# Kernel optimization log

Hardware: AMD Instinct MI355X
Metric: run time of the kernel (lower is better)

Reference implementation:

```python
import jax, jax.numpy as jnp
import numpy as np

N_NODES = 500000   # total temporal-graph nodes (memory slots)
N_SUB = 50000      # nodes in sampled subgraph (|n_id|)
E = 500000         # edges from LastNeighborLoader (N_SUB * neighbor_size)
B = 5000           # events in the batch
D = 100            # memory_dim == embedding_dim
TD = 100           # time_dim
MSG = 100          # msg_dim
H = 2              # TransformerConv heads
C = D // H         # per-head channels
OUT = 100          # predictor out_channels


def setup_inputs() -> dict:
    key = jax.random.key(0)
    ks = jax.random.split(key, 32)
    s = 0.1
    r = lambda i, shp: jax.random.normal(ks[i], shp, dtype=jnp.float32) * s
    return {
        'memory': r(0, (N_NODES, D)),
        'last_update': jax.random.randint(ks[1], (N_NODES,), 0, 1000000, dtype=jnp.int32),
        'n_id': jax.random.randint(ks[2], (N_SUB,), 0, N_NODES, dtype=jnp.int32),
        'edge_index': jax.random.randint(ks[3], (2, E), 0, N_SUB, dtype=jnp.int32),
        't': jax.random.randint(ks[4], (E,), 0, 1000000, dtype=jnp.int32),
        'msg': r(5, (E, MSG)),
        'src_idx': jax.random.randint(ks[6], (B,), 0, N_SUB, dtype=jnp.int32),
        'dst_idx': jax.random.randint(ks[7], (B,), 0, N_SUB, dtype=jnp.int32),
        'w_time': r(8, (TD, 1)), 'b_time': r(9, (TD,)),
        'Wq': r(10, (D, H * C)), 'bq': r(11, (H * C,)),
        'Wk': r(12, (D, H * C)), 'bk': r(13, (H * C,)),
        'Wv': r(14, (D, H * C)), 'bv': r(15, (H * C,)),
        'We': r(16, (MSG + TD, H * C)),
        'Wskip': r(17, (D, H * C)), 'bskip': r(18, (H * C,)),
        'Wps': r(19, (D, D)), 'bps': r(20, (D,)),
        'Wpd': r(21, (D, D)), 'bpd': r(22, (D,)),
        'Wpf': r(23, (D, OUT)), 'bpf': r(24, (OUT,)),
    }


def reference(memory, last_update, n_id, edge_index, t, msg, src_idx, dst_idx,
              w_time, b_time, Wq, bq, Wk, bk, Wv, bv, We, Wskip, bskip,
              Wps, bps, Wpd, bpd, Wpf, bpf):
    # --- memory lookup: z, last_update = memory(n_id) ---
    z = memory[n_id]                       # [N_SUB, D] gather
    lu = last_update[n_id]                 # [N_SUB]

    src = edge_index[0]
    dst = edge_index[1]

    # --- relative time encoding: cos(Linear(1, time_dim)) ---
    rel_t = (lu[src] - t).astype(jnp.float32)              # [E]
    rel_t_enc = jnp.cos(rel_t[:, None] * w_time[:, 0][None, :] + b_time)  # [E, TD]
    edge_attr = jnp.concatenate([rel_t_enc, msg], axis=-1)  # [E, TD+MSG]

    # --- TransformerConv (heads=H, per-head C, edge_dim, root skip) ---
    q = (z @ Wq + bq).reshape(N_SUB, H, C)
    k = (z @ Wk + bk).reshape(N_SUB, H, C)
    v = (z @ Wv + bv).reshape(N_SUB, H, C)
    e = (edge_attr @ We).reshape(E, H, C)

    key_e = k[src] + e                     # [E, H, C]
    val_e = v[src] + e                     # [E, H, C]
    alpha = jnp.sum(q[dst] * key_e, axis=-1) / jnp.sqrt(jnp.float32(C))  # [E, H]

    # segment softmax over incoming edges of each dst node
    m = jax.ops.segment_max(alpha, dst, num_segments=N_SUB)   # [N_SUB, H]
    a = jnp.exp(alpha - m[dst])
    denom = jax.ops.segment_sum(a, dst, num_segments=N_SUB)
    a = a / (denom[dst] + 1e-16)

    agg = jax.ops.segment_sum(a[:, :, None] * val_e, dst, num_segments=N_SUB)  # [N_SUB, H, C]
    out = agg.reshape(N_SUB, H * C) + (z @ Wskip + bskip)     # [N_SUB, D]

    # --- predictor on src/dst embeddings (assoc remap already applied) ---
    h = jax.nn.relu((out[src_idx] @ Wps + bps) + (out[dst_idx] @ Wpd + bpd))
    pred = h @ Wpf + bpf                   # [B, OUT]
    return pred
```

## Files before the change

kernel.cpp:

```cpp
#include <hip/hip_runtime.h>
#include <math.h>

#define N_SUBN  50000
#define NE      500000
#define NB      5000
#define NL      (2*NB)
#define DDIM    100
#define TDIM    100
#define KATTR   200
#define NCHUNK  49

typedef __attribute__((ext_vector_type(8))) short short8;
typedef __attribute__((ext_vector_type(4))) float f32x4;

__device__ inline unsigned short f2bf(float f){
  union{float f; unsigned int u;} v; v.f = f;
  unsigned int r = (v.u + 0x7fffu + ((v.u >> 16) & 1u)) >> 16;
  return (unsigned short)r;
}
__device__ inline float bf2f(unsigned short u){
  union{unsigned int u; float f;} v; v.u = ((unsigned int)u) << 16;
  return v.f;
}

__device__ inline float fast_cos(float x){
  constexpr double TWO_PI_D = 6.2831853071795864769252867665590;
  constexpr float I2PI = (float)(1.0/TWO_PI_D);
  constexpr float C1 = (float)TWO_PI_D;
  constexpr float C2 = (float)(TWO_PI_D - (double)((float)TWO_PI_D));
  float k = rintf(x * I2PI);
  float r = fmaf(k, -C1, x);
  r = fmaf(k, -C2, r);
  return __cosf(r);
}

__global__ __launch_bounds__(256) void k_misc(
    const int* __restrict__ lastu, const int* __restrict__ nid,
    int* __restrict__ cnt, int* __restrict__ mark, int* __restrict__ lusub,
    const float* __restrict__ We,
    const float* __restrict__ Wq, const float* __restrict__ Wk,
    const float* __restrict__ Wv, const float* __restrict__ Ws,
    const float* __restrict__ Wps, const float* __restrict__ Wpd,
    const float* __restrict__ Wpf,
    unsigned short* __restrict__ Wnb, unsigned short* __restrict__ Wqxb,
    unsigned short* __restrict__ Wfb)
{
  int i = blockIdx.x*256 + threadIdx.x;
  if (i < N_SUBN){
    cnt[i] = 0;
    mark[i] = 0;
    lusub[i] = lastu[nid[i]];
  }
  if (i < 7*28*64){
    int l = i & 63; int t = i >> 6;
    int which = t / 28; int t2 = t - which*28;
    int kt = t2 / 7; int nt = t2 - kt*7;
    const float* W = (which==0)?Wq:(which==1)?Wk:(which==2)?Wv:(which==3)?Ws:
                     (which==4)?Wps:(which==5)?Wpd:Wpf;
    int col = nt*16 + (l & 15);
    int kbase = kt*32 + ((l >> 4) << 3);
    short8 pack;
    #pragma unroll
    for (int j = 0; j < 8; ++j){
      int k = kbase + j;
      float v = (k < DDIM && col < DDIM) ? W[k*DDIM + col] : 0.f;
      pack[j] = (short)f2bf(v);
    }
    *((short8*)Wnb + i) = pack;
  }
  if (i < 4*25*64){
    int l = i & 63; int t = i >> 6;
    int kt = t / 25; int nt = t - kt*25;
    int col = nt*16 + (l & 15);
    int h = col / 200; int d = col - h*200;
    int kbase = kt*32 + ((l >> 4) << 3);
    short8 pack;
    #pragma unroll
    for (int j = 0; j < 8; ++j){
      int k = kbase + j;
      float v = (k >= h*50 && k < h*50 + 50) ? We[d*DDIM + k] : 0.f;
      pack[j] = (short)f2bf(v);
    }
    *((short8*)Wqxb + i) = pack;
  }
  if (i < 13*7*64){
    int l = i & 63; int t = i >> 6;
    int kt = t / 7; int nt = t - kt*7;
    int col = nt*16 + (l & 15);
    int kbase = kt*32 + ((l >> 4) << 3);
    short8 pack;
    #pragma unroll
    for (int j = 0; j < 8; ++j){
      int k = kbase + j;
      float v = 0.f;
      if (col < DDIM && k < 2*KATTR){
        int h = col / 50; int blk = k / KATTR; int d = k - blk*KATTR;
        v = (blk == h) ? We[d*DDIM + col] : 0.f;
      }
      pack[j] = (short)f2bf(v);
    }
    *((short8*)Wfb + i) = pack;
  }
}

__global__ void k_mark(const int* __restrict__ srci, const int* __restrict__ dsti,
                       int* __restrict__ mark){
  int i = blockIdx.x*blockDim.x + threadIdx.x;
  if (i < NB){
    mark[srci[i]] = 1;
    mark[dsti[i]] = 1;
  }
}

__global__ void k_hist(const int* __restrict__ ei, const int* __restrict__ mark,
                       int* __restrict__ cnt){
  int i = blockIdx.x*blockDim.x + threadIdx.x;
  if (i < NE){
    int d = ei[NE + i];
    if (mark[d]) atomicAdd(&cnt[d], 1);
  }
}

__global__ __launch_bounds__(256) void k_bsum(const int* __restrict__ cnt, int* __restrict__ bsum){
  __shared__ int wsum[4];
  int b = blockIdx.x, tid = threadIdx.x;
  int base = b*1024 + tid*4;
  int s = 0;
  #pragma unroll
  for (int i=0;i<4;i++){ int idx = base+i; if (idx < N_SUBN) s += cnt[idx]; }
  #pragma unroll
  for (int m=1;m<64;m<<=1) s += __shfl_xor(s, m);
  if ((tid&63)==0) wsum[tid>>6] = s;
  __syncthreads();
  if (tid==0) bsum[b] = wsum[0]+wsum[1]+wsum[2]+wsum[3];
}

__global__ void k_bscan(const int* __restrict__ bsum, int* __restrict__ bbase){
  int l = threadIdx.x;
  int v = (l < NCHUNK) ? bsum[l] : 0;
  int orig = v;
  for (int off=1; off<64; off<<=1){
    int t = __shfl_up(v, off);
    if (l >= off) v += t;
  }
  if (l < NCHUNK) bbase[l] = v - orig;
}

__global__ __launch_bounds__(1024) void k_off(const int* __restrict__ cnt, const int* __restrict__ bbase,
                                              int* __restrict__ rowptr, int* __restrict__ ofs){
  __shared__ int sd[1024];
  int b = blockIdx.x, tid = threadIdx.x;
  int i = b*1024 + tid;
  int v = (i < N_SUBN) ? cnt[i] : 0;
  sd[tid] = v; __syncthreads();
  for (int off=1; off<1024; off<<=1){
    int t = (tid >= off) ? sd[tid-off] : 0;
    __syncthreads();
    sd[tid] += t;
    __syncthreads();
  }
  int incl = sd[tid] + bbase[b];
  if (i < N_SUBN){ rowptr[i+1] = incl; ofs[i] = incl - v; }
  if (i == 0) rowptr[0] = 0;
}

__global__ void k_perm(const int* __restrict__ ei, const int* __restrict__ tt,
                       const int* __restrict__ lusub, const int* __restrict__ mark,
                       int* __restrict__ ofs, uint4* __restrict__ spr){
  int i = blockIdx.x*blockDim.x + threadIdx.x;
  if (i < NE){
    int d = ei[NE + i];
    if (mark[d]){
      int s = ei[i];
      float rel = (float)(lusub[s] - tt[i]);
      int pos = atomicAdd(&ofs[d], 1);
      spr[pos] = make_uint4((unsigned)s, (unsigned)i, __float_as_uint(rel), 0u);
    }
  }
}

__global__ __launch_bounds__(256, 4) void k_nodeKV(
    const float* __restrict__ mem, const int* __restrict__ nid,
    const unsigned short* __restrict__ Wnb,
    const float* __restrict__ bk, const float* __restrict__ bv,
    unsigned short* __restrict__ kvb)
{
  const int tid = threadIdx.x;
  const int lane = tid & 63;
  const int w = tid >> 6;
  const int node0 = blockIdx.x*64;
  const int arow = w*16 + (lane & 15);
  const int koff = (lane >> 4) << 3;

  int node = node0 + arow;
  int nc = (node < N_SUBN) ? node : (N_SUBN-1);
  const float* zrow = mem + (size_t)nid[nc]*DDIM;

  f32x4 ak[7], av[7];
  #pragma unroll
  for (int nt=0; nt<7; ++nt){ ak[nt] = (f32x4){0,0,0,0}; av[nt] = (f32x4){0,0,0,0}; }

  #pragma unroll
  for (int kt=0; kt<4; ++kt){
    const int k0 = kt*32 + koff;
    short8 a;
    if (k0 + 7 < DDIM){
      float4 m0 = *(const float4*)(zrow + k0);
      float4 m1 = *(const float4*)(zrow + k0 + 4);
      a[0] = (short)f2bf(m0.x); a[1] = (short)f2bf(m0.y);
      a[2] = (short)f2bf(m0.z); a[3] = (short)f2bf(m0.w);
      a[4] = (short)f2bf(m1.x); a[5] = (short)f2bf(m1.y);
      a[6] = (short)f2bf(m1.z); a[7] = (short)f2bf(m1.w);
    } else if (k0 >= DDIM){
      #pragma unroll
      for (int j=0;j<8;++j) a[j] = 0;
    } else {
      float4 m0 = *(const float4*)(zrow + 96);
      a[0] = (short)f2bf(m0.x); a[1] = (short)f2bf(m0.y);
      a[2] = (short)f2bf(m0.z); a[3] = (short)f2bf(m0.w);
      a[4] = 0; a[5] = 0; a[6] = 0; a[7] = 0;
    }
    const short8* wk = (const short8*)Wnb + (size_t)((1*4 + kt)*7)*64 + lane;
    const short8* wv = (const short8*)Wnb + (size_t)((2*4 + kt)*7)*64 + lane;
    #pragma unroll
    for (int nt=0; nt<7; ++nt){
      ak[nt] = __builtin_amdgcn_mfma_f32_16x16x32_bf16(a, wk[(size_t)nt*64], ak[nt], 0, 0, 0);
      av[nt] = __builtin_amdgcn_mfma_f32_16x16x32_bf16(a, wv[(size_t)nt*64], av[nt], 0, 0, 0);
    }
  }

  const int colb = lane & 15;
  const int rbase = w*16 + ((lane >> 4) << 2);
  #pragma unroll
  for (int nt=0; nt<7; ++nt){
    int col = nt*16 + colb;
    if (col >= DDIM) continue;
    float bbk = bk[col], bbv = bv[col];
    #pragma unroll
    for (int r=0; r<4; ++r){
      int nn = node0 + rbase + r;
      if (nn < N_SUBN){
        unsigned pk = (unsigned)f2bf(ak[nt][r] + bbk)
                    | ((unsigned)f2bf(av[nt][r] + bbv) << 16);
        *(unsigned*)(kvb + (size_t)nn*(2*DDIM) + col*2) = pk;
      }
    }
  }
}

__global__ __launch_bounds__(256, 4) void k_nodeQS(
    const float* __restrict__ mem, const int* __restrict__ nid,
    const int* __restrict__ srci, const int* __restrict__ dsti,
    const unsigned short* __restrict__ Wnb,
    const float* __restrict__ bq, const float* __restrict__ bs,
    float* __restrict__ qs, float* __restrict__ ss)
{
  const int tid = threadIdx.x;
  const int lane = tid & 63;
  const int w = tid >> 6;
  const int i0 = blockIdx.x*64;
  const int arow = w*16 + (lane & 15);
  const int koff = (lane >> 4) << 3;

  int idx = i0 + arow;
  int idxc = (idx < NL) ? idx : (NL-1);
  int node = (idxc < NB) ? srci[idxc] : dsti[idxc - NB];
  const float* zrow = mem + (size_t)nid[node]*DDIM;

  f32x4 aq[7], as_[7];
  #pragma unroll
  for (int nt=0; nt<7; ++nt){ aq[nt] = (f32x4){0,0,0,0}; as_[nt] = (f32x4){0,0,0,0}; }

  #pragma unroll
  for (int kt=0; kt<4; ++kt){
    const int k0 = kt*32 + koff;
    short8 a;
    if (k0 + 7 < DDIM){
      float4 m0 = *(const float4*)(zrow + k0);
      float4 m1 = *(const float4*)(zrow + k0 + 4);
      a[0] = (short)f2bf(m0.x); a[1] = (short)f2bf(m0.y);
      a[2] = (short)f2bf(m0.z); a[3] = (short)f2bf(m0.w);
      a[4] = (short)f2bf(m1.x); a[5] = (short)f2bf(m1.y);
      a[6] = (short)f2bf(m1.z); a[7] = (short)f2bf(m1.w);
    } else if (k0 >= DDIM){
      #pragma unroll
      for (int j=0;j<8;++j) a[j] = 0;
    } else {
      float4 m0 = *(const float4*)(zrow + 96);
      a[0] = (short)f2bf(m0.x); a[1] = (short)f2bf(m0.y);
      a[2] = (short)f2bf(m0.z); a[3] = (short)f2bf(m0.w);
      a[4] = 0; a[5] = 0; a[6] = 0; a[7] = 0;
    }
    const short8* wq = (const short8*)Wnb + (size_t)((0*4 + kt)*7)*64 + lane;
    const short8* ws = (const short8*)Wnb + (size_t)((3*4 + kt)*7)*64 + lane;
    #pragma unroll
    for (int nt=0; nt<7; ++nt){
      aq[nt]  = __builtin_amdgcn_mfma_f32_16x16x32_bf16(a, wq[(size_t)nt*64], aq[nt], 0, 0, 0);
      as_[nt] = __builtin_amdgcn_mfma_f32_16x16x32_bf16(a, ws[(size_t)nt*64], as_[nt], 0, 0, 0);
    }
  }

  const int colb = lane & 15;
  const int rbase = w*16 + ((lane >> 4) << 2);
  int nd[4]; bool on[4];
  #pragma unroll
  for (int r=0; r<4; ++r){
    int ii = i0 + rbase + r;
    on[r] = ii < NL;
    int iic = on[r] ? ii : (NL-1);
    nd[r] = (iic < NB) ? srci[iic] : dsti[iic - NB];
  }
  #pragma unroll
  for (int nt=0; nt<7; ++nt){
    int col = nt*16 + colb;
    if (col >= DDIM) continue;
    float bbq = bq[col], bbs = bs[col];
    #pragma unroll
    for (int r=0; r<4; ++r){
      if (on[r]){
        qs[(size_t)nd[r]*DDIM + col] = aq[nt][r] + bbq;
        ss[(size_t)nd[r]*DDIM + col] = as_[nt][r] + bbs;
      }
    }
  }
}

__global__ __launch_bounds__(256) void k_qex(
    const float* __restrict__ qs, const int* __restrict__ srci, const int* __restrict__ dsti,
    const unsigned short* __restrict__ Wqxb, unsigned short* __restrict__ qexb)
{
  const int tid = threadIdx.x;
  const int lane = tid & 63;
  const int w = tid >> 6;
  const int i0 = blockIdx.x*64;
  const int arow = w*16 + (lane & 15);
  const int koff = (lane >> 4) << 3;

  int idx = i0 + arow;
  int idxc = (idx < NL) ? idx : (NL-1);
  int node = (idxc < NB) ? srci[idxc] : dsti[idxc - NB];
  const float* qrow = qs + (size_t)node*DDIM;

  f32x4 acc[25];
  #pragma unroll
  for (int nt=0; nt<25; ++nt) acc[nt] = (f32x4){0,0,0,0};

  #pragma unroll
  for (int kt=0; kt<4; ++kt){
    const int k0 = kt*32 + koff;
    short8 a;
    if (k0 + 7 < DDIM){
      float4 m0 = *(const float4*)(qrow + k0);
      float4 m1 = *(const float4*)(qrow + k0 + 4);
      a[0] = (short)f2bf(m0.x); a[1] = (short)f2bf(m0.y);
      a[2] = (short)f2bf(m0.z); a[3] = (short)f2bf(m0.w);
      a[4] = (short)f2bf(m1.x); a[5] = (short)f2bf(m1.y);
      a[6] = (short)f2bf(m1.z); a[7] = (short)f2bf(m1.w);
    } else if (k0 >= DDIM){
      #pragma unroll
      for (int j=0;j<8;++j) a[j] = 0;
    } else {
      float4 m0 = *(const float4*)(qrow + 96);
      a[0] = (short)f2bf(m0.x); a[1] = (short)f2bf(m0.y);
      a[2] = (short)f2bf(m0.z); a[3] = (short)f2bf(m0.w);
      a[4] = 0; a[5] = 0; a[6] = 0; a[7] = 0;
    }
    const short8* wb = (const short8*)Wqxb + (size_t)(kt*25)*64 + lane;
    #pragma unroll
    for (int nt=0; nt<25; ++nt){
      short8 b = wb[(size_t)nt*64];
      acc[nt] = __builtin_amdgcn_mfma_f32_16x16x32_bf16(a, b, acc[nt], 0, 0, 0);
    }
  }

  const int colb = lane & 15;
  const int rbase = w*16 + ((lane >> 4) << 2);
  int nd[4]; bool on[4];
  #pragma unroll
  for (int r=0; r<4; ++r){
    int ii = i0 + rbase + r;
    on[r] = ii < NL;
    int iic = on[r] ? ii : (NL-1);
    nd[r] = (iic < NB) ? srci[iic] : dsti[iic - NB];
  }
  #pragma unroll
  for (int nt=0; nt<25; ++nt){
    int col = nt*16 + colb;
    #pragma unroll
    for (int r=0; r<4; ++r){
      if (on[r]) qexb[(size_t)nd[r]*400 + col] = f2bf(acc[nt][r]);
    }
  }
}

__global__ __launch_bounds__(256) void k_agg(
    const int* __restrict__ rowptr, const uint4* __restrict__ spr,
    const int* __restrict__ srci, const int* __restrict__ dsti,
    const float* __restrict__ msg, const float* __restrict__ qs,
    const unsigned short* __restrict__ qexb, const unsigned short* __restrict__ kvb,
    const float* __restrict__ wt, const float* __restrict__ bt,
    unsigned short* __restrict__ sbarb, float* __restrict__ numvb,
    float* __restrict__ denb)
{
  const int w = __builtin_amdgcn_readfirstlane(threadIdx.x >> 6);
  const int lane = threadIdx.x & 63;
  const int idx = blockIdx.x*4 + w;
  const int node = (idx < NB) ? srci[idx] : dsti[idx - NB];
  const bool act = lane < 50;
  const int l = lane;
  const float INV = 0.14142135623730951f;

  float wtA=0,wtB=0,btA=0,btB=0,q0=0,q1=0;
  float qx0=0,qx1=0,qx2=0,qx3=0,qx4=0,qx5=0,qx6=0,qx7=0;
  if (act){
    wtA = wt[l]; wtB = wt[50+l]; btA = bt[l]; btB = bt[50+l];
    q0 = qs[(size_t)node*DDIM + l]; q1 = qs[(size_t)node*DDIM + 50 + l];
    const unsigned short* qe = qexb + (size_t)node*400;
    qx0 = bf2f(qe[l]);      qx1 = bf2f(qe[50+l]);
    qx2 = bf2f(qe[100+l]);  qx3 = bf2f(qe[150+l]);
    qx4 = bf2f(qe[200+l]);  qx5 = bf2f(qe[250+l]);
    qx6 = bf2f(qe[300+l]);  qx7 = bf2f(qe[350+l]);
  }
  const int b0 = rowptr[node], b1 = rowptr[node+1];
  float den0=0.f, den1=0.f, nv0=0.f, nv1=0.f;
  float sb0=0.f,sb1=0.f,sb2=0.f,sb3=0.f,sb4=0.f,sb5=0.f,sb6=0.f,sb7=0.f;

  const int nE = b1 - b0;
  const int npairs = nE >> 1;

  uint4 sA = make_uint4(0,0,0,0), sB = sA, nsA = sA, nsB = sA;
  float mAA=0,mBA=0,mAB=0,mBB=0;
  unsigned pA0=0,pA1=0,pB0=0,pB1=0;

  if (npairs > 0){
    sA = spr[b0]; sB = spr[b0+1];
    if (act){
      mAA = msg[(size_t)sA.y*DDIM + l];  mBA = msg[(size_t)sA.y*DDIM + 50 + l];
      mAB = msg[(size_t)sB.y*DDIM + l];  mBB = msg[(size_t)sB.y*DDIM + 50 + l];
      pA0 = *(const unsigned*)(kvb + (size_t)sA.x*(2*DDIM) + 2*l);
      pA1 = *(const unsigned*)(kvb + (size_t)sA.x*(2*DDIM) + 100 + 2*l);
      pB0 = *(const unsigned*)(kvb + (size_t)sB.x*(2*DDIM) + 2*l);
      pB1 = *(const unsigned*)(kvb + (size_t)sB.x*(2*DDIM) + 100 + 2*l);
    }
    if (npairs > 1){ nsA = spr[b0+2]; nsB = spr[b0+3]; }
  }

  for (int j = 0; j < npairs; ++j){
    float nmAA=0,nmBA=0,nmAB=0,nmBB=0;
    unsigned npA0=0,npA1=0,npB0=0,npB1=0;
    if (j+1 < npairs && act){
      nmAA = msg[(size_t)nsA.y*DDIM + l];  nmBA = msg[(size_t)nsA.y*DDIM + 50 + l];
      nmAB = msg[(size_t)nsB.y*DDIM + l];  nmBB = msg[(size_t)nsB.y*DDIM + 50 + l];
      npA0 = *(const unsigned*)(kvb + (size_t)nsA.x*(2*DDIM) + 2*l);
      npA1 = *(const unsigned*)(kvb + (size_t)nsA.x*(2*DDIM) + 100 + 2*l);
      npB0 = *(const unsigned*)(kvb + (size_t)nsB.x*(2*DDIM) + 2*l);
      npB1 = *(const unsigned*)(kvb + (size_t)nsB.x*(2*DDIM) + 100 + 2*l);
    }
    uint4 nnsA = nsA, nnsB = nsB;
    if (j+2 < npairs){
      nnsA = spr[b0 + 2*(j+2)];
      nnsB = spr[b0 + 2*(j+2) + 1];
    }

    float relA = __uint_as_float(sA.z);
    float relB = __uint_as_float(sB.z);
    float cAA=0,cBA=0,cAB=0,cBB=0;
    float kA0=0,vA0=0,kA1=0,vA1=0,kB0=0,vB0=0,kB1=0,vB1=0;
    if (act){
      kA0 = bf2f((unsigned short)(pA0 & 0xffff)); vA0 = bf2f((unsigned short)(pA0 >> 16));
      kA1 = bf2f((unsigned short)(pA1 & 0xffff)); vA1 = bf2f((unsigned short)(pA1 >> 16));
      kB0 = bf2f((unsigned short)(pB0 & 0xffff)); vB0 = bf2f((unsigned short)(pB0 >> 16));
      kB1 = bf2f((unsigned short)(pB1 & 0xffff)); vB1 = bf2f((unsigned short)(pB1 >> 16));
      cAA = fast_cos(__fadd_rn(__fmul_rn(relA, wtA), btA));
// ... 212 lines not shown
      hl[rbase + r][col] = fmaxf(acc[nt][r] + bbias, 0.f);
  }
  __syncthreads();

  f32x4 ac2[7];
  #pragma unroll
  for (int nt=0; nt<7; ++nt) ac2[nt] = (f32x4){0,0,0,0};

  #pragma unroll
  for (int kt=0; kt<4; ++kt){
    const int k0 = kt*32 + koff;
    short8 a;
    if (k0 + 7 < DDIM){
      float4 h0 = *(const float4*)(&hl[arow][k0]);
      float4 h1 = *(const float4*)(&hl[arow][k0 + 4]);
      a[0]=(short)f2bf(h0.x); a[1]=(short)f2bf(h0.y); a[2]=(short)f2bf(h0.z); a[3]=(short)f2bf(h0.w);
      a[4]=(short)f2bf(h1.x); a[5]=(short)f2bf(h1.y); a[6]=(short)f2bf(h1.z); a[7]=(short)f2bf(h1.w);
    } else if (k0 >= DDIM){
      #pragma unroll
      for (int j=0;j<8;++j) a[j] = 0;
    } else {
      float4 h0 = *(const float4*)(&hl[arow][96]);
      a[0]=(short)f2bf(h0.x); a[1]=(short)f2bf(h0.y); a[2]=(short)f2bf(h0.z); a[3]=(short)f2bf(h0.w);
      a[4]=0; a[5]=0; a[6]=0; a[7]=0;
    }
    const short8* wpf = (const short8*)Wnb + (size_t)((6*4 + kt)*7)*64 + lane;
    #pragma unroll
    for (int nt=0; nt<7; ++nt)
      ac2[nt] = __builtin_amdgcn_mfma_f32_16x16x32_bf16(a, wpf[(size_t)nt*64], ac2[nt], 0, 0, 0);
  }

  #pragma unroll
  for (int nt=0; nt<7; ++nt){
    int col = nt*16 + colb;
    if (col >= DDIM) continue;
    float bb = bpf[col];
    #pragma unroll
    for (int r=0; r<4; ++r){
      int bo = bb0 + rbase + r;
      if (bo < NB) outp[(size_t)bo*DDIM + col] = ac2[nt][r] + bb;
    }
  }
}

extern "C" void kernel_launch(void* const* d_in, const int* in_sizes, int n_in,
                              void* d_out, int out_size, void* d_ws, size_t ws_size,
                              hipStream_t stream)
{
  const float* mem   = (const float*)d_in[0];
  const int*   lastu = (const int*)  d_in[1];
  const int*   nid   = (const int*)  d_in[2];
  const int*   ei    = (const int*)  d_in[3];
  const int*   tt    = (const int*)  d_in[4];
  const float* msg   = (const float*)d_in[5];
  const int*   srci  = (const int*)  d_in[6];
  const int*   dsti  = (const int*)  d_in[7];
  const float* wtime = (const float*)d_in[8];
  const float* btime = (const float*)d_in[9];
  const float* Wq = (const float*)d_in[10]; const float* bq = (const float*)d_in[11];
  const float* Wk = (const float*)d_in[12]; const float* bk = (const float*)d_in[13];
  const float* Wv = (const float*)d_in[14]; const float* bv = (const float*)d_in[15];
  const float* We = (const float*)d_in[16];
  const float* Ws = (const float*)d_in[17]; const float* bs = (const float*)d_in[18];
  const float* Wps= (const float*)d_in[19]; const float* bps= (const float*)d_in[20];
  const float* Wpd= (const float*)d_in[21]; const float* bpd= (const float*)d_in[22];
  const float* Wpf= (const float*)d_in[23]; const float* bpf= (const float*)d_in[24];

  char* wsp = (char*)d_ws;
  auto alloc = [&](size_t bytes)->void*{
    void* p = (void*)wsp;
    wsp += (bytes + 255) & ~(size_t)255;
    return p;
  };
  float* qs   = (float*)alloc((size_t)N_SUBN*DDIM*4);
  unsigned short* kvb  = (unsigned short*)alloc((size_t)N_SUBN*DDIM*2*2);
  float* ssb  = (float*)alloc((size_t)N_SUBN*DDIM*4);
  float* oute = (float*)alloc((size_t)N_SUBN*DDIM*4);
  unsigned short* qexb = (unsigned short*)alloc((size_t)N_SUBN*400*2);
  unsigned short* sbarb= (unsigned short*)alloc((size_t)N_SUBN*400*2);
  float* numvb= (float*)alloc((size_t)N_SUBN*DDIM*4);
  float* denb = (float*)alloc((size_t)N_SUBN*2*4);
  int* cnt    = (int*)alloc((size_t)N_SUBN*4);
  int* mark   = (int*)alloc((size_t)N_SUBN*4);
  int* rowptr = (int*)alloc((size_t)(N_SUBN+1)*4);
  int* ofs    = (int*)alloc((size_t)N_SUBN*4);
  int* bsum   = (int*)alloc((size_t)NCHUNK*4);
  int* bbase  = (int*)alloc((size_t)NCHUNK*4);
  uint4* spr  = (uint4*)alloc((size_t)NE*16);
  int* lusub  = (int*)alloc((size_t)N_SUBN*4);
  unsigned short* Wnb  = (unsigned short*)alloc((size_t)7*28*64*8*2);
  unsigned short* Wqxb = (unsigned short*)alloc((size_t)4*25*64*8*2);
  unsigned short* Wfb  = (unsigned short*)alloc((size_t)13*7*64*8*2);

  k_misc<<<(N_SUBN+255)/256, 256, 0, stream>>>(lastu, nid, cnt, mark, lusub, We,
                                               Wq, Wk, Wv, Ws, Wps, Wpd, Wpf,
                                               Wnb, Wqxb, Wfb);
  k_mark<<<(NB+255)/256, 256, 0, stream>>>(srci, dsti, mark);
  k_hist<<<(NE+255)/256, 256, 0, stream>>>(ei, mark, cnt);
  k_bsum<<<NCHUNK, 256, 0, stream>>>(cnt, bsum);
  k_bscan<<<1, 64, 0, stream>>>(bsum, bbase);
  k_off<<<NCHUNK, 1024, 0, stream>>>(cnt, bbase, rowptr, ofs);
  k_perm<<<(NE+255)/256, 256, 0, stream>>>(ei, tt, lusub, mark, ofs, spr);

  k_nodeKV<<<(N_SUBN+63)/64, 256, 0, stream>>>(mem, nid, Wnb, bk, bv, kvb);
  k_nodeQS<<<(NL+63)/64, 256, 0, stream>>>(mem, nid, srci, dsti, Wnb, bq, bs, qs, ssb);
  k_qex<<<(NL+63)/64, 256, 0, stream>>>(qs, srci, dsti, Wqxb, qexb);

  k_agg<<<NL/4, 256, 0, stream>>>(rowptr, spr, srci, dsti, msg, qs,
                                  qexb, kvb, wtime, btime,
                                  sbarb, numvb, denb);

  k_final<<<(NL+63)/64, 256, 0, stream>>>(sbarb, Wfb, srci, dsti, numvb, denb, ssb, oute);

  k_pred<<<(NB+63)/64, 256, 0, stream>>>(oute, srci, dsti, Wnb, bps, bpd, bpf,
                                         (float*)d_out);
}
```

Before: 145.1 us.

## Fold Wq into We projection, skip unneeded KV nodes, merge scan kernels

Precomputes the product of Wq and the per-head We slices, plus a combined bias, so the query-times-edge-weight projection is computed straight from memory rows. This fuses the q/skip projection and the qex projection into one kernel. It also marks source nodes of edges that feed batch destinations, and skips the memory loads and K/V stores for all other nodes. The separate block-scan kernel is removed by having each k_off block sum the preceding block totals itself. The trade-offs are fewer launches and less gather traffic against a serial 50-term dot product per element in the setup kernel and higher register pressure in the fused kernel.

```diff
diff --git a/kernel.cpp b/kernel.cpp
--- a/kernel.cpp
+++ b/kernel.cpp
@@ -36,19 +36,21 @@
 
 __global__ __launch_bounds__(256) void k_misc(
     const int* __restrict__ lastu, const int* __restrict__ nid,
-    int* __restrict__ cnt, int* __restrict__ mark, int* __restrict__ lusub,
+    int* __restrict__ cnt, int* __restrict__ mark, int* __restrict__ mark2,
+    int* __restrict__ lusub,
     const float* __restrict__ We,
     const float* __restrict__ Wq, const float* __restrict__ Wk,
     const float* __restrict__ Wv, const float* __restrict__ Ws,
     const float* __restrict__ Wps, const float* __restrict__ Wpd,
-    const float* __restrict__ Wpf,
-    unsigned short* __restrict__ Wnb, unsigned short* __restrict__ Wqxb,
-    unsigned short* __restrict__ Wfb)
+    const float* __restrict__ Wpf, const float* __restrict__ bq,
+    unsigned short* __restrict__ Wnb, unsigned short* __restrict__ Wqxcb,
+    unsigned short* __restrict__ Wfb, float* __restrict__ bcomb)
 {
   int i = blockIdx.x*256 + threadIdx.x;
   if (i < N_SUBN){
     cnt[i] = 0;
     mark[i] = 0;
+    mark2[i] = 0;
     lusub[i] = lastu[nid[i]];
   }
   if (i < 7*28*64){
@@ -76,12 +78,25 @@
     int kbase = kt*32 + ((l >> 4) << 3);
     short8 pack;
     #pragma unroll
-    for (int j = 0; j < 8; ++j){
-      int k = kbase + j;
-      float v = (k >= h*50 && k < h*50 + 50) ? We[d*DDIM + k] : 0.f;
-      pack[j] = (short)f2bf(v);
-    }
-    *((short8*)Wqxb + i) = pack;
+    for (int j8 = 0; j8 < 8; ++j8){
+      int k = kbase + j8;
+      float v = 0.f;
+      if (k < DDIM){
+        const float* wqr = Wq + k*DDIM + h*50;
+        const float* wer = We + d*DDIM + h*50;
+        for (int j = 0; j < 50; ++j) v = fmaf(wqr[j], wer[j], v);
+      }
+      pack[j8] = (short)f2bf(v);
+    }
+    *((short8*)Wqxcb + i) = pack;
+  }
+  if (i < 400){
+    int h = i / 200; int d = i - h*200;
+    const float* wer = We + d*DDIM + h*50;
+    const float* bqr = bq + h*50;
+    float v = 0.f;
+    for (int j = 0; j < 50; ++j) v = fmaf(bqr[j], wer[j], v);
+    bcomb[i] = v;
   }
   if (i < 13*7*64){
     int l = i & 63; int t = i >> 6;
@@ -113,11 +128,14 @@
 }
 
 __global__ void k_hist(const int* __restrict__ ei, const int* __restrict__ mark,
-                       int* __restrict__ cnt){
+                       int* __restrict__ cnt, int* __restrict__ mark2){
   int i = blockIdx.x*blockDim.x + threadIdx.x;
   if (i < NE){
     int d = ei[NE + i];
-    if (mark[d]) atomicAdd(&cnt[d], 1);
+    if (mark[d]){
+      atomicAdd(&cnt[d], 1);
+      mark2[ei[i]] = 1;
+    }
   }
 }
 
@@ -135,21 +153,17 @@
   if (tid==0) bsum[b] = wsum[0]+wsum[1]+wsum[2]+wsum[3];
 }
 
-__global__ void k_bscan(const int* __restrict__ bsum, int* __restrict__ bbase){
-  int l = threadIdx.x;
-  int v = (l < NCHUNK) ? bsum[l] : 0;
-  int orig = v;
-  for (int off=1; off<64; off<<=1){
-    int t = __shfl_up(v, off);
-    if (l >= off) v += t;
-  }
-  if (l < NCHUNK) bbase[l] = v - orig;
-}
-
-__global__ __launch_bounds__(1024) void k_off(const int* __restrict__ cnt, const int* __restrict__ bbase,
+__global__ __launch_bounds__(1024) void k_off(const int* __restrict__ cnt, const int* __restrict__ bsum,
                                               int* __restrict__ rowptr, int* __restrict__ ofs){
   __shared__ int sd[1024];
+  __shared__ int sbb;
   int b = blockIdx.x, tid = threadIdx.x;
+  if (tid < 64){
+    int v = (tid < b) ? bsum[tid] : 0;
+    #pragma unroll
+    for (int m=1;m<64;m<<=1) v += __shfl_xor(v, m);
+    if (tid == 0) sbb = v;
+  }
   int i = b*1024 + tid;
   int v = (i < N_SUBN) ? cnt[i] : 0;
   sd[tid] = v; __syncthreads();
@@ -159,7 +173,7 @@
     sd[tid] += t;
     __syncthreads();
   }
-  int incl = sd[tid] + bbase[b];
+  int incl = sd[tid] + sbb;
   if (i < N_SUBN){ rowptr[i+1] = incl; ofs[i] = incl - v; }
   if (i == 0) rowptr[0] = 0;
 }
@@ -181,6 +195,7 @@
 
 __global__ __launch_bounds__(256, 4) void k_nodeKV(
     const float* __restrict__ mem, const int* __restrict__ nid,
+    const int* __restrict__ mark2,
     const unsigned short* __restrict__ Wnb,
     const float* __restrict__ bk, const float* __restrict__ bv,
     unsigned short* __restrict__ kvb)
@@ -194,11 +209,93 @@
 
   int node = node0 + arow;
   int nc = (node < N_SUBN) ? node : (N_SUBN-1);
+  const bool need = (node < N_SUBN) && mark2[nc];
   const float* zrow = mem + (size_t)nid[nc]*DDIM;
 
   f32x4 ak[7], av[7];
   #pragma unroll
   for (int nt=0; nt<7; ++nt){ ak[nt] = (f32x4){0,0,0,0}; av[nt] = (f32x4){0,0,0,0}; }
+
+  #pragma unroll
+  for (int kt=0; kt<4; ++kt){
+    const int k0 = kt*32 + koff;
+    short8 a;
+    #pragma unroll
+    for (int j=0;j<8;++j) a[j] = 0;
+    if (need){
+      if (k0 + 7 < DDIM){
+        float4 m0 = *(const float4*)(zrow + k0);
+        float4 m1 = *(const float4*)(zrow + k0 + 4);
+        a[0] = (short)f2bf(m0.x); a[1] = (short)f2bf(m0.y);
+        a[2] = (short)f2bf(m0.z); a[3] = (short)f2bf(m0.w);
+        a[4] = (short)f2bf(m1.x); a[5] = (short)f2bf(m1.y);
+        a[6] = (short)f2bf(m1.z); a[7] = (short)f2bf(m1.w);
+      } else if (k0 < DDIM){
+        float4 m0 = *(const float4*)(zrow + 96);
+        a[0] = (short)f2bf(m0.x); a[1] = (short)f2bf(m0.y);
+        a[2] = (short)f2bf(m0.z); a[3] = (short)f2bf(m0.w);
+      }
+    }
+    const short8* wk = (const short8*)Wnb + (size_t)((1*4 + kt)*7)*64 + lane;
+    const short8* wv = (const short8*)Wnb + (size_t)((2*4 + kt)*7)*64 + lane;
+    #pragma unroll
+    for (int nt=0; nt<7; ++nt){
+      ak[nt] = __builtin_amdgcn_mfma_f32_16x16x32_bf16(a, wk[(size_t)nt*64], ak[nt], 0, 0, 0);
+      av[nt] = __builtin_amdgcn_mfma_f32_16x16x32_bf16(a, wv[(size_t)nt*64], av[nt], 0, 0, 0);
+    }
+  }
+
+  const int colb = lane & 15;
+  const int rbase = w*16 + ((lane >> 4) << 2);
+  int nn0 = node0 + rbase;
+  int m2[4];
+  #pragma unroll
+  for (int r=0; r<4; ++r){
+    int nn = nn0 + r;
+    m2[r] = (nn < N_SUBN) ? mark2[nn] : 0;
+  }
+  #pragma unroll
+  for (int nt=0; nt<7; ++nt){
+    int col = nt*16 + colb;
+    if (col >= DDIM) continue;
+    float bbk = bk[col], bbv = bv[col];
+    #pragma unroll
+    for (int r=0; r<4; ++r){
+      if (m2[r]){
+        int nn = nn0 + r;
+        unsigned pk = (unsigned)f2bf(ak[nt][r] + bbk)
+                    | ((unsigned)f2bf(av[nt][r] + bbv) << 16);
+        *(unsigned*)(kvb + (size_t)nn*(2*DDIM) + col*2) = pk;
+      }
+    }
+  }
+}
+
+__global__ __launch_bounds__(256, 2) void k_nodeQSX(
+    const float* __restrict__ mem, const int* __restrict__ nid,
+    const int* __restrict__ srci, const int* __restrict__ dsti,
+    const unsigned short* __restrict__ Wnb, const unsigned short* __restrict__ Wqxcb,
+    const float* __restrict__ bq, const float* __restrict__ bs,
+    const float* __restrict__ bcomb,
+    float* __restrict__ qs, float* __restrict__ ss, unsigned short* __restrict__ qexb)
+{
+  const int tid = threadIdx.x;
+  const int lane = tid & 63;
+  const int w = tid >> 6;
+  const int i0 = blockIdx.x*64;
+  const int arow = w*16 + (lane & 15);
+  const int koff = (lane >> 4) << 3;
+
+  int idx = i0 + arow;
+  int idxc = (idx < NL) ? idx : (NL-1);
+  int node = (idxc < NB) ? srci[idxc] : dsti[idxc - NB];
+  const float* zrow = mem + (size_t)nid[node]*DDIM;
+
+  f32x4 aq[7], as_[7], ax[25];
+  #pragma unroll
+  for (int nt=0; nt<7; ++nt){ aq[nt] = (f32x4){0,0,0,0}; as_[nt] = (f32x4){0,0,0,0}; }
+  #pragma unroll
+  for (int nt=0; nt<25; ++nt) ax[nt] = (f32x4){0,0,0,0};
 
   #pragma unroll
   for (int kt=0; kt<4; ++kt){
@@ -220,84 +317,17 @@
       a[2] = (short)f2bf(m0.z); a[3] = (short)f2bf(m0.w);
       a[4] = 0; a[5] = 0; a[6] = 0; a[7] = 0;
     }
-    const short8* wk = (const short8*)Wnb + (size_t)((1*4 + kt)*7)*64 + lane;
-    const short8* wv = (const short8*)Wnb + (size_t)((2*4 + kt)*7)*64 + lane;
-    #pragma unroll
-    for (int nt=0; nt<7; ++nt){
-      ak[nt] = __builtin_amdgcn_mfma_f32_16x16x32_bf16(a, wk[(size_t)nt*64], ak[nt], 0, 0, 0);
-      av[nt] = __builtin_amdgcn_mfma_f32_16x16x32_bf16(a, wv[(size_t)nt*64], av[nt], 0, 0, 0);
-    }
-  }
-
-  const int colb = lane & 15;
-  const int rbase = w*16 + ((lane >> 4) << 2);
-  #pragma unroll
-  for (int nt=0; nt<7; ++nt){
-    int col = nt*16 + colb;
-    if (col >= DDIM) continue;
-    float bbk = bk[col], bbv = bv[col];
-    #pragma unroll
-    for (int r=0; r<4; ++r){
-      int nn = node0 + rbase + r;
-      if (nn < N_SUBN){
-        unsigned pk = (unsigned)f2bf(ak[nt][r] + bbk)
-                    | ((unsigned)f2bf(av[nt][r] + bbv) << 16);
-        *(unsigned*)(kvb + (size_t)nn*(2*DDIM) + col*2) = pk;
-      }
-    }
-  }
-}
-
-__global__ __launch_bounds__(256, 4) void k_nodeQS(
-    const float* __restrict__ mem, const int* __restrict__ nid,
-    const int* __restrict__ srci, const int* __restrict__ dsti,
-    const unsigned short* __restrict__ Wnb,
-    const float* __restrict__ bq, const float* __restrict__ bs,
-    float* __restrict__ qs, float* __restrict__ ss)
-{
-  const int tid = threadIdx.x;
-  const int lane = tid & 63;
-  const int w = tid >> 6;
-  const int i0 = blockIdx.x*64;
-  const int arow = w*16 + (lane & 15);
-  const int koff = (lane >> 4) << 3;
-
-  int idx = i0 + arow;
-  int idxc = (idx < NL) ? idx : (NL-1);
-  int node = (idxc < NB) ? srci[idxc] : dsti[idxc - NB];
-  const float* zrow = mem + (size_t)nid[node]*DDIM;
-
-  f32x4 aq[7], as_[7];
-  #pragma unroll
-  for (int nt=0; nt<7; ++nt){ aq[nt] = (f32x4){0,0,0,0}; as_[nt] = (f32x4){0,0,0,0}; }
-
-  #pragma unroll
-  for (int kt=0; kt<4; ++kt){
-    const int k0 = kt*32 + koff;
-    short8 a;
-    if (k0 + 7 < DDIM){
-      float4 m0 = *(const float4*)(zrow + k0);
-      float4 m1 = *(const float4*)(zrow + k0 + 4);
-      a[0] = (short)f2bf(m0.x); a[1] = (short)f2bf(m0.y);
-      a[2] = (short)f2bf(m0.z); a[3] = (short)f2bf(m0.w);
-      a[4] = (short)f2bf(m1.x); a[5] = (short)f2bf(m1.y);
-      a[6] = (short)f2bf(m1.z); a[7] = (short)f2bf(m1.w);
-    } else if (k0 >= DDIM){
-      #pragma unroll
-      for (int j=0;j<8;++j) a[j] = 0;
-    } else {
-      float4 m0 = *(const float4*)(zrow + 96);
-      a[0] = (short)f2bf(m0.x); a[1] = (short)f2bf(m0.y);
-      a[2] = (short)f2bf(m0.z); a[3] = (short)f2bf(m0.w);
-      a[4] = 0; a[5] = 0; a[6] = 0; a[7] = 0;
-    }
     const short8* wq = (const short8*)Wnb + (size_t)((0*4 + kt)*7)*64 + lane;
     const short8* ws = (const short8*)Wnb + (size_t)((3*4 + kt)*7)*64 + lane;
+    const short8* wx = (const short8*)Wqxcb + (size_t)(kt*25)*64 + lane;
     #pragma unroll
     for (int nt=0; nt<7; ++nt){
       aq[nt]  = __builtin_amdgcn_mfma_f32_16x16x32_bf16(a, wq[(size_t)nt*64], aq[nt], 0, 0, 0);
       as_[nt] = __builtin_amdgcn_mfma_f32_16x16x32_bf16(a, ws[(size_t)nt*64], as_[nt], 0, 0, 0);
     }
+    #pragma unroll
+    for (int nt=0; nt<25; ++nt)
+      ax[nt] = __builtin_amdgcn_mfma_f32_16x16x32_bf16(a, wx[(size_t)nt*64], ax[nt], 0, 0, 0);
   }
 
   const int colb = lane & 15;
@@ -323,72 +353,13 @@
       }
     }
   }
-}
-
-__global__ __launch_bounds__(256) void k_qex(
-    const float* __restrict__ qs, const int* __restrict__ srci, const int* __restrict__ dsti,
-    const unsigned short* __restrict__ Wqxb, unsigned short* __restrict__ qexb)
-{
-  const int tid = threadIdx.x;
-  const int lane = tid & 63;
-  const int w = tid >> 6;
-  const int i0 = blockIdx.x*64;
-  const int arow = w*16 + (lane & 15);
-  const int koff = (lane >> 4) << 3;
-
-  int idx = i0 + arow;
-  int idxc = (idx < NL) ? idx : (NL-1);
-  int node = (idxc < NB) ? srci[idxc] : dsti[idxc - NB];
-  const float* qrow = qs + (size_t)node*DDIM;
-
-  f32x4 acc[25];
-  #pragma unroll
-  for (int nt=0; nt<25; ++nt) acc[nt] = (f32x4){0,0,0,0};
-
-  #pragma unroll
-  for (int kt=0; kt<4; ++kt){
-    const int k0 = kt*32 + koff;
-    short8 a;
-    if (k0 + 7 < DDIM){
-      float4 m0 = *(const float4*)(qrow + k0);
-      float4 m1 = *(const float4*)(qrow + k0 + 4);
-      a[0] = (short)f2bf(m0.x); a[1] = (short)f2bf(m0.y);
-      a[2] = (short)f2bf(m0.z); a[3] = (short)f2bf(m0.w);
-      a[4] = (short)f2bf(m1.x); a[5] = (short)f2bf(m1.y);
-      a[6] = (short)f2bf(m1.z); a[7] = (short)f2bf(m1.w);
-    } else if (k0 >= DDIM){
-      #pragma unroll
-      for (int j=0;j<8;++j) a[j] = 0;
-    } else {
-      float4 m0 = *(const float4*)(qrow + 96);
-      a[0] = (short)f2bf(m0.x); a[1] = (short)f2bf(m0.y);
-      a[2] = (short)f2bf(m0.z); a[3] = (short)f2bf(m0.w);
-      a[4] = 0; a[5] = 0; a[6] = 0; a[7] = 0;
-    }
-    const short8* wb = (const short8*)Wqxb + (size_t)(kt*25)*64 + lane;
-    #pragma unroll
-    for (int nt=0; nt<25; ++nt){
-      short8 b = wb[(size_t)nt*64];
-      acc[nt] = __builtin_amdgcn_mfma_f32_16x16x32_bf16(a, b, acc[nt], 0, 0, 0);
-    }
-  }
-
-  const int colb = lane & 15;
-  const int rbase = w*16 + ((lane >> 4) << 2);
-  int nd[4]; bool on[4];
-  #pragma unroll
-  for (int r=0; r<4; ++r){
-    int ii = i0 + rbase + r;
-    on[r] = ii < NL;
-    int iic = on[r] ? ii : (NL-1);
-    nd[r] = (iic < NB) ? srci[iic] : dsti[iic - NB];
-  }
   #pragma unroll
   for (int nt=0; nt<25; ++nt){
     int col = nt*16 + colb;
+    float bc = bcomb[col];
     #pragma unroll
     for (int r=0; r<4; ++r){
-      if (on[r]) qexb[(size_t)nd[r]*400 + col] = f2bf(acc[nt][r]);
+      if (on[r]) qexb[(size_t)nd[r]*400 + col] = f2bf(ax[nt][r] + bc);
     }
   }
 }
@@ -767,29 +738,29 @@
   float* denb = (float*)alloc((size_t)N_SUBN*2*4);
   int* cnt    = (int*)alloc((size_t)N_SUBN*4);
   int* mark   = (int*)alloc((size_t)N_SUBN*4);
+  int* mark2  = (int*)alloc((size_t)N_SUBN*4);
   int* rowptr = (int*)alloc((size_t)(N_SUBN+1)*4);
   int* ofs    = (int*)alloc((size_t)N_SUBN*4);
   int* bsum   = (int*)alloc((size_t)NCHUNK*4);
-  int* bbase  = (int*)alloc((size_t)NCHUNK*4);
   uint4* spr  = (uint4*)alloc((size_t)NE*16);
   int* lusub  = (int*)alloc((size_t)N_SUBN*4);
-  unsigned short* Wnb  = (unsigned short*)alloc((size_t)7*28*64*8*2);
-  unsigned short* Wqxb = (unsigned short*)alloc((size_t)4*25*64*8*2);
-  unsigned short* Wfb  = (unsigned short*)alloc((size_t)13*7*64*8*2);
-
-  k_misc<<<(N_SUBN+255)/256, 256, 0, stream>>>(lastu, nid, cnt, mark, lusub, We,
-                                               Wq, Wk, Wv, Ws, Wps, Wpd, Wpf,
-                                               Wnb, Wqxb, Wfb);
+  unsigned short* Wnb   = (unsigned short*)alloc((size_t)7*28*64*8*2);
+  unsigned short* Wqxcb = (unsigned short*)alloc((size_t)4*25*64*8*2);
+  unsigned short* Wfb   = (unsigned short*)alloc((size_t)13*7*64*8*2);
+  float* bcomb = (float*)alloc((size_t)400*4);
+
+  k_misc<<<(N_SUBN+255)/256, 256, 0, stream>>>(lastu, nid, cnt, mark, mark2, lusub, We,
+                                               Wq, Wk, Wv, Ws, Wps, Wpd, Wpf, bq,
+                                               Wnb, Wqxcb, Wfb, bcomb);
   k_mark<<<(NB+255)/256, 256, 0, stream>>>(srci, dsti, mark);
-  k_hist<<<(NE+255)/256, 256, 0, stream>>>(ei, mark, cnt);
+  k_hist<<<(NE+255)/256, 256, 0, stream>>>(ei, mark, cnt, mark2);
   k_bsum<<<NCHUNK, 256, 0, stream>>>(cnt, bsum);
-  k_bscan<<<1, 64, 0, stream>>>(bsum, bbase);
-  k_off<<<NCHUNK, 1024, 0, stream>>>(cnt, bbase, rowptr, ofs);
+  k_off<<<NCHUNK, 1024, 0, stream>>>(cnt, bsum, rowptr, ofs);
   k_perm<<<(NE+255)/256, 256, 0, stream>>>(ei, tt, lusub, mark, ofs, spr);
 
-  k_nodeKV<<<(N_SUBN+63)/64, 256, 0, stream>>>(mem, nid, Wnb, bk, bv, kvb);
-  k_nodeQS<<<(NL+63)/64, 256, 0, stream>>>(mem, nid, srci, dsti, Wnb, bq, bs, qs, ssb);
-  k_qex<<<(NL+63)/64, 256, 0, stream>>>(qs, srci, dsti, Wqxb, qexb);
+  k_nodeKV<<<(N_SUBN+63)/64, 256, 0, stream>>>(mem, nid, mark2, Wnb, bk, bv, kvb);
+  k_nodeQSX<<<(NL+63)/64, 256, 0, stream>>>(mem, nid, srci, dsti, Wnb, Wqxcb,
+                                            bq, bs, bcomb, qs, ssb, qexb);
 
   k_agg<<<NL/4, 256, 0, stream>>>(rowptr, spr, srci, dsti, msg, qs,
                                   qexb, kvb, wtime, btime,
```

Result: slower. 159.7 us (+10.0%).

## Skip K/V projection for nodes never used as sources of needed edges

Applied to the files above, without the earlier changes.

Marks, during the histogram pass, every source node of an edge whose destination is a predictor endpoint. The K/V node projection then loads memory rows and writes K/V only for those marked nodes, cutting gather traffic and stores for unused nodes. Separately, the single-block chunk scan kernel is removed and each offset block computes its own base from the chunk sums, saving one launch. MFMA work still runs for every tile, so compute is unchanged; only memory traffic shrinks.

```diff
diff --git a/kernel.cpp b/kernel.cpp
--- a/kernel.cpp
+++ b/kernel.cpp
@@ -36,7 +36,8 @@
 
 __global__ __launch_bounds__(256) void k_misc(
     const int* __restrict__ lastu, const int* __restrict__ nid,
-    int* __restrict__ cnt, int* __restrict__ mark, int* __restrict__ lusub,
+    int* __restrict__ cnt, int* __restrict__ mark, int* __restrict__ mark2,
+    int* __restrict__ lusub,
     const float* __restrict__ We,
     const float* __restrict__ Wq, const float* __restrict__ Wk,
     const float* __restrict__ Wv, const float* __restrict__ Ws,
@@ -49,6 +50,7 @@
   if (i < N_SUBN){
     cnt[i] = 0;
     mark[i] = 0;
+    mark2[i] = 0;
     lusub[i] = lastu[nid[i]];
   }
   if (i < 7*28*64){
@@ -113,11 +115,14 @@
 }
 
 __global__ void k_hist(const int* __restrict__ ei, const int* __restrict__ mark,
-                       int* __restrict__ cnt){
+                       int* __restrict__ cnt, int* __restrict__ mark2){
   int i = blockIdx.x*blockDim.x + threadIdx.x;
   if (i < NE){
     int d = ei[NE + i];
-    if (mark[d]) atomicAdd(&cnt[d], 1);
+    if (mark[d]){
+      atomicAdd(&cnt[d], 1);
+      mark2[ei[i]] = 1;
+    }
   }
 }
 
@@ -135,21 +140,17 @@
   if (tid==0) bsum[b] = wsum[0]+wsum[1]+wsum[2]+wsum[3];
 }
 
-__global__ void k_bscan(const int* __restrict__ bsum, int* __restrict__ bbase){
-  int l = threadIdx.x;
-  int v = (l < NCHUNK) ? bsum[l] : 0;
-  int orig = v;
-  for (int off=1; off<64; off<<=1){
-    int t = __shfl_up(v, off);
-    if (l >= off) v += t;
-  }
-  if (l < NCHUNK) bbase[l] = v - orig;
-}
-
-__global__ __launch_bounds__(1024) void k_off(const int* __restrict__ cnt, const int* __restrict__ bbase,
+__global__ __launch_bounds__(1024) void k_off(const int* __restrict__ cnt, const int* __restrict__ bsum,
                                               int* __restrict__ rowptr, int* __restrict__ ofs){
   __shared__ int sd[1024];
+  __shared__ int sbb;
   int b = blockIdx.x, tid = threadIdx.x;
+  if (tid < 64){
+    int v = (tid < b) ? bsum[tid] : 0;
+    #pragma unroll
+    for (int m=1;m<64;m<<=1) v += __shfl_xor(v, m);
+    if (tid == 0) sbb = v;
+  }
   int i = b*1024 + tid;
   int v = (i < N_SUBN) ? cnt[i] : 0;
   sd[tid] = v; __syncthreads();
@@ -159,7 +160,7 @@
     sd[tid] += t;
     __syncthreads();
   }
-  int incl = sd[tid] + bbase[b];
+  int incl = sd[tid] + sbb;
   if (i < N_SUBN){ rowptr[i+1] = incl; ofs[i] = incl - v; }
   if (i == 0) rowptr[0] = 0;
 }
@@ -181,6 +182,7 @@
 
 __global__ __launch_bounds__(256, 4) void k_nodeKV(
     const float* __restrict__ mem, const int* __restrict__ nid,
+    const int* __restrict__ mark2,
     const unsigned short* __restrict__ Wnb,
     const float* __restrict__ bk, const float* __restrict__ bv,
     unsigned short* __restrict__ kvb)
@@ -194,6 +196,7 @@
 
   int node = node0 + arow;
   int nc = (node < N_SUBN) ? node : (N_SUBN-1);
+  const bool need = (node < N_SUBN) && mark2[nc];
   const float* zrow = mem + (size_t)nid[nc]*DDIM;
 
   f32x4 ak[7], av[7];
@@ -204,21 +207,21 @@
   for (int kt=0; kt<4; ++kt){
     const int k0 = kt*32 + koff;
     short8 a;
-    if (k0 + 7 < DDIM){
-      float4 m0 = *(const float4*)(zrow + k0);
-      float4 m1 = *(const float4*)(zrow + k0 + 4);
-      a[0] = (short)f2bf(m0.x); a[1] = (short)f2bf(m0.y);
-      a[2] = (short)f2bf(m0.z); a[3] = (short)f2bf(m0.w);
-      a[4] = (short)f2bf(m1.x); a[5] = (short)f2bf(m1.y);
-      a[6] = (short)f2bf(m1.z); a[7] = (short)f2bf(m1.w);
-    } else if (k0 >= DDIM){
-      #pragma unroll
-      for (int j=0;j<8;++j) a[j] = 0;
-    } else {
-      float4 m0 = *(const float4*)(zrow + 96);
-      a[0] = (short)f2bf(m0.x); a[1] = (short)f2bf(m0.y);
-      a[2] = (short)f2bf(m0.z); a[3] = (short)f2bf(m0.w);
-      a[4] = 0; a[5] = 0; a[6] = 0; a[7] = 0;
+    #pragma unroll
+    for (int j=0;j<8;++j) a[j] = 0;
+    if (need){
+      if (k0 + 7 < DDIM){
+        float4 m0 = *(const float4*)(zrow + k0);
+        float4 m1 = *(const float4*)(zrow + k0 + 4);
+        a[0] = (short)f2bf(m0.x); a[1] = (short)f2bf(m0.y);
+        a[2] = (short)f2bf(m0.z); a[3] = (short)f2bf(m0.w);
+        a[4] = (short)f2bf(m1.x); a[5] = (short)f2bf(m1.y);
+        a[6] = (short)f2bf(m1.z); a[7] = (short)f2bf(m1.w);
+      } else if (k0 < DDIM){
+        float4 m0 = *(const float4*)(zrow + 96);
+        a[0] = (short)f2bf(m0.x); a[1] = (short)f2bf(m0.y);
+        a[2] = (short)f2bf(m0.z); a[3] = (short)f2bf(m0.w);
+      }
     }
     const short8* wk = (const short8*)Wnb + (size_t)((1*4 + kt)*7)*64 + lane;
     const short8* wv = (const short8*)Wnb + (size_t)((2*4 + kt)*7)*64 + lane;
@@ -231,6 +234,13 @@
 
   const int colb = lane & 15;
   const int rbase = w*16 + ((lane >> 4) << 2);
+  int nn0 = node0 + rbase;
+  int m2[4];
+  #pragma unroll
+  for (int r=0; r<4; ++r){
+    int nn = nn0 + r;
+    m2[r] = (nn < N_SUBN) ? mark2[nn] : 0;
+  }
   #pragma unroll
   for (int nt=0; nt<7; ++nt){
     int col = nt*16 + colb;
@@ -238,8 +248,8 @@
     float bbk = bk[col], bbv = bv[col];
     #pragma unroll
     for (int r=0; r<4; ++r){
-      int nn = node0 + rbase + r;
-      if (nn < N_SUBN){
+      if (m2[r]){
+        int nn = nn0 + r;
         unsigned pk = (unsigned)f2bf(ak[nt][r] + bbk)
                     | ((unsigned)f2bf(av[nt][r] + bbv) << 16);
         *(unsigned*)(kvb + (size_t)nn*(2*DDIM) + col*2) = pk;
@@ -767,27 +777,26 @@
   float* denb = (float*)alloc((size_t)N_SUBN*2*4);
   int* cnt    = (int*)alloc((size_t)N_SUBN*4);
   int* mark   = (int*)alloc((size_t)N_SUBN*4);
+  int* mark2  = (int*)alloc((size_t)N_SUBN*4);
   int* rowptr = (int*)alloc((size_t)(N_SUBN+1)*4);
   int* ofs    = (int*)alloc((size_t)N_SUBN*4);
   int* bsum   = (int*)alloc((size_t)NCHUNK*4);
-  int* bbase  = (int*)alloc((size_t)NCHUNK*4);
   uint4* spr  = (uint4*)alloc((size_t)NE*16);
   int* lusub  = (int*)alloc((size_t)N_SUBN*4);
   unsigned short* Wnb  = (unsigned short*)alloc((size_t)7*28*64*8*2);
   unsigned short* Wqxb = (unsigned short*)alloc((size_t)4*25*64*8*2);
   unsigned short* Wfb  = (unsigned short*)alloc((size_t)13*7*64*8*2);
 
-  k_misc<<<(N_SUBN+255)/256, 256, 0, stream>>>(lastu, nid, cnt, mark, lusub, We,
+  k_misc<<<(N_SUBN+255)/256, 256, 0, stream>>>(lastu, nid, cnt, mark, mark2, lusub, We,
                                                Wq, Wk, Wv, Ws, Wps, Wpd, Wpf,
                                                Wnb, Wqxb, Wfb);
   k_mark<<<(NB+255)/256, 256, 0, stream>>>(srci, dsti, mark);
-  k_hist<<<(NE+255)/256, 256, 0, stream>>>(ei, mark, cnt);
+  k_hist<<<(NE+255)/256, 256, 0, stream>>>(ei, mark, cnt, mark2);
   k_bsum<<<NCHUNK, 256, 0, stream>>>(cnt, bsum);
-  k_bscan<<<1, 64, 0, stream>>>(bsum, bbase);
-  k_off<<<NCHUNK, 1024, 0, stream>>>(cnt, bbase, rowptr, ofs);
+  k_off<<<NCHUNK, 1024, 0, stream>>>(cnt, bsum, rowptr, ofs);
   k_perm<<<(NE+255)/256, 256, 0, stream>>>(ei, tt, lusub, mark, ofs, spr);
 
-  k_nodeKV<<<(N_SUBN+63)/64, 256, 0, stream>>>(mem, nid, Wnb, bk, bv, kvb);
+  k_nodeKV<<<(N_SUBN+63)/64, 256, 0, stream>>>(mem, nid, mark2, Wnb, bk, bv, kvb);
   k_nodeQS<<<(NL+63)/64, 256, 0, stream>>>(mem, nid, srci, dsti, Wnb, bq, bs, qs, ssb);
   k_qex<<<(NL+63)/64, 256, 0, stream>>>(qs, srci, dsti, Wqxb, qexb);
 
```

Result: no change. 144.7 us (-0.3%).
